# Performance work log

Measured on AMD Instinct MI355X. Metric: run time of the kernel, lower is better.

Reference implementation:

```python
import jax, jax.numpy as jnp
import numpy as np

DIM = 256
NUM_HEADS = 4
HEAD_DIM = DIM // NUM_HEADS
LN_EPS = 1e-5


def setup_inputs() -> dict:
    key = jax.random.key(0)
    ks = jax.random.split(key, 5)
    B, C, H, W = 4, DIM, 64, 64
    x = jax.random.normal(ks[0], (B, C, H, W), dtype=jnp.float32)
    ln_g = jnp.ones((DIM,), dtype=jnp.float32)
    ln_b = jnp.zeros((DIM,), dtype=jnp.float32)
    # torch Linear init scale ~ 1/sqrt(fan_in)
    w_qkv = jax.random.normal(ks[1], (DIM, 3 * DIM), dtype=jnp.float32) / np.sqrt(DIM)
    w_proj = jax.random.normal(ks[2], (DIM, DIM), dtype=jnp.float32) / np.sqrt(DIM)
    b_proj = jax.random.normal(ks[3], (DIM,), dtype=jnp.float32) * 0.01
    return {"x": x, "ln_g": ln_g, "ln_b": ln_b, "w_qkv": w_qkv,
            "w_proj": w_proj, "b_proj": b_proj}


def _attention_block(x, ln_g, ln_b, w_qkv, w_proj, b_proj):
    B, C, H, W = x.shape
    N = H * W
    h, d = NUM_HEADS, HEAD_DIM
    # b c h w -> b n c
    t = x.reshape(B, C, N).transpose(0, 2, 1)
    # LayerNorm over channel dim
    mu = jnp.mean(t, axis=-1, keepdims=True)
    var = jnp.mean(jnp.square(t - mu), axis=-1, keepdims=True)
    t = (t - mu) * jax.lax.rsqrt(var + LN_EPS) * ln_g + ln_b
    # qkv projection (no bias); layout of last dim is (three, heads, d)
    qkv = t @ w_qkv  # [B, N, 3*C]
    qkv = qkv.reshape(B, N, 3, h, d)
    q = qkv[:, :, 0].transpose(0, 2, 1, 3)  # [B, h, N, d]
    k = qkv[:, :, 1].transpose(0, 2, 1, 3)
    v = qkv[:, :, 2].transpose(0, 2, 1, 3)
    # scaled dot-product attention (original chunks over queries; same math)
    scale = 1.0 / jnp.sqrt(jnp.asarray(d, dtype=q.dtype))
    dots = jnp.einsum('bhnd,bhmd->bhnm', q, k) * scale
    attn = jax.nn.softmax(dots, axis=-1)
    o = jnp.einsum('bhnm,bhmd->bhnd', attn, v)  # [B, h, N, d]
    # b h n d -> b n (h d)
    o = o.transpose(0, 2, 1, 3).reshape(B, N, C)
    o = o @ w_proj.T + b_proj  # torch Linear convention not needed; keep explicit
    # b n c -> b c h w
    return o.transpose(0, 2, 1).reshape(B, C, H, W)


def reference(x, ln_g, ln_b, w_qkv, w_proj, b_proj):
    return _attention_block(x, ln_g, ln_b, w_qkv, w_proj, b_proj)
```

## Files before the change

kernel.cpp:

```cpp
#include <hip/hip_runtime.h>
#include <math.h>

#define NB 4
#define NC 256
#define NHEADS 4
#define DH 64
#define NT 4096
#define QSCALE (0.125f * 1.44269504088896f)

typedef __bf16  bf16x8 __attribute__((ext_vector_type(8)));
typedef __bf16  bf16x4 __attribute__((ext_vector_type(4)));
typedef float   f32x4  __attribute__((ext_vector_type(4)));
typedef short   s16x8  __attribute__((ext_vector_type(8)));

static __device__ __forceinline__ unsigned short f2bf(float f) {
    unsigned u = __float_as_uint(f);
    u = (u + 0x7fffu + ((u >> 16) & 1u)) >> 16;
    return (unsigned short)u;
}

static __device__ __forceinline__ void gload16(const unsigned short* g, unsigned short* l) {
    __builtin_amdgcn_global_load_lds((const __attribute__((address_space(1))) void*)g,
                                     (__attribute__((address_space(3))) void*)l, 16, 0, 0);
}

static __device__ __forceinline__ void stage_64x256(
    unsigned short* __restrict__ lds, const unsigned short* __restrict__ g, int tid)
{
    #pragma unroll
    for (int chunk = 0; chunk < 8; ++chunk) {
        const int row = chunk * 8 + (tid >> 5);
        const int col = (tid & 31) * 8;
        *(s16x8*)&lds[row * 264 + col] = *(const s16x8*)&g[row * 256 + col];
    }
}

__global__ __launch_bounds__(256) void k_prep(
    const float* __restrict__ wqkv, const float* __restrict__ wproj,
    unsigned short* __restrict__ wqkv_t, unsigned short* __restrict__ wproj_bf)
{
    const int id = blockIdx.x;
    const int tid = threadIdx.x;
    if (id < 48) {
        __shared__ float T[64][65];
        const int jt = id % 12, ct = id / 12;
        #pragma unroll
        for (int p = 0; p < 16; ++p) {
            const int idx = tid + (p << 8);
            const int r = idx >> 6, cl = idx & 63;
            T[r][cl] = wqkv[(size_t)(ct * 64 + r) * 768 + jt * 64 + cl];
        }
        __syncthreads();
        #pragma unroll
        for (int p = 0; p < 16; ++p) {
            const int idx = tid + (p << 8);
            const int r = idx >> 6, cl = idx & 63;
            wqkv_t[(size_t)(jt * 64 + r) * 256 + ct * 64 + cl] = f2bf(T[cl][r]);
        }
    } else {
        const int base = (id - 48) * 2048 + tid * 8;
        s16x8 v;
        #pragma unroll
        for (int j = 0; j < 8; ++j) v[j] = (short)f2bf(wproj[base + j]);
        *(s16x8*)&wproj_bf[base] = v;
    }
}

__global__ __launch_bounds__(256) void k_ln_qkv(
    const float* __restrict__ x,
    const float* __restrict__ ln_g,
    const float* __restrict__ ln_b,
    const unsigned short* __restrict__ wqkv_t,
    unsigned short* __restrict__ q_bf,
    unsigned short* __restrict__ k_bf,
    unsigned short* __restrict__ v_bf)
{
    __shared__ unsigned short An[64 * 264];
    __shared__ unsigned short Wt[64 * 264];
    __shared__ float red1[4][64], red2[4][64];
    __shared__ float mu_s[64], rs_s[64];

    const int b     = blockIdx.x >> 6;
    const int n0    = (blockIdx.x & 63) << 6;
    const int three = blockIdx.y;
    const int tid   = threadIdx.x;
    const int li    = tid & 63;
    const int grp   = tid >> 6;
    const int w     = grp;
    const int lane  = li;
    const int q4    = lane >> 4;
    const int c     = lane & 15;

    const float* xb = x + ((size_t)b * NC) * NT + n0 + li;

    float xr[64];
    #pragma unroll
    for (int chunk = 0; chunk < 8; ++chunk)
        #pragma unroll
        for (int j = 0; j < 8; ++j)
            xr[chunk * 8 + j] = xb[(size_t)(chunk * 32 + grp * 8 + j) * NT];

    float s1 = 0.f, s2 = 0.f;
    #pragma unroll
    for (int i = 0; i < 64; ++i) { s1 += xr[i]; s2 += xr[i] * xr[i]; }
    red1[grp][li] = s1; red2[grp][li] = s2;
    __syncthreads();
    if (tid < 64) {
        const float t1 = red1[0][tid] + red1[1][tid] + red1[2][tid] + red1[3][tid];
        const float t2 = red2[0][tid] + red2[1][tid] + red2[2][tid] + red2[3][tid];
        const float mu  = t1 * (1.0f / NC);
        const float var = t2 * (1.0f / NC) - mu * mu;
        mu_s[tid] = mu;
        rs_s[tid] = rsqrtf(var + 1e-5f);
    }
    __syncthreads();
    const float mu = mu_s[li];
    const float rs = rs_s[li];

    #pragma unroll
    for (int chunk = 0; chunk < 8; ++chunk) {
        s16x8 pk;
        #pragma unroll
        for (int j = 0; j < 8; ++j) {
            const int ch = chunk * 32 + grp * 8 + j;
            const float vv = (xr[chunk * 8 + j] - mu) * rs * ln_g[ch] + ln_b[ch];
            pk[j] = (short)f2bf(vv);
        }
        *(s16x8*)&An[li * 264 + chunk * 32 + grp * 8] = pk;
    }
    __syncthreads();

    bf16x8 aT[8];
    if (three < 2) {
        #pragma unroll
        for (int kt = 0; kt < 8; ++kt)
            aT[kt] = *(const bf16x8*)&An[(16 * w + c) * 264 + kt * 32 + q4 * 8];
    }

    for (int jt = 0; jt < 4; ++jt) {
        __syncthreads();
        stage_64x256(Wt, wqkv_t + (size_t)(three * 256 + jt * 64) * 256, tid);
        __syncthreads();

        f32x4 acc[4];
        #pragma unroll
        for (int nt = 0; nt < 4; ++nt)
            #pragma unroll
            for (int r = 0; r < 4; ++r) acc[nt][r] = 0.f;

        const int bh = b * NHEADS + jt;
        if (three < 2) {
            #pragma unroll
            for (int nt = 0; nt < 4; ++nt)
                #pragma unroll
                for (int kt = 0; kt < 8; ++kt) {
                    const bf16x8 bb = *(const bf16x8*)&Wt[(16 * nt + c) * 264 + kt * 32 + q4 * 8];
                    acc[nt] = __builtin_amdgcn_mfma_f32_16x16x32_bf16(aT[kt], bb, acc[nt], 0, 0, 0);
                }
            unsigned short* dst = (three == 0 ? q_bf : k_bf) + ((size_t)bh * NT + n0) * DH;
            const float sc = (three == 0) ? QSCALE : 1.0f;
            #pragma unroll
            for (int nt = 0; nt < 4; ++nt)
                #pragma unroll
                for (int r = 0; r < 4; ++r)
                    dst[(size_t)(16 * w + 4 * q4 + r) * DH + 16 * nt + c] = f2bf(acc[nt][r] * sc);
        } else {
            bf16x8 aW[8];
            #pragma unroll
            for (int kt = 0; kt < 8; ++kt)
                aW[kt] = *(const bf16x8*)&Wt[(16 * w + c) * 264 + kt * 32 + q4 * 8];
            #pragma unroll
            for (int nt = 0; nt < 4; ++nt)
                #pragma unroll
                for (int kt = 0; kt < 8; ++kt) {
                    const bf16x8 bb = *(const bf16x8*)&An[(16 * nt + c) * 264 + kt * 32 + q4 * 8];
                    acc[nt] = __builtin_amdgcn_mfma_f32_16x16x32_bf16(aW[kt], bb, acc[nt], 0, 0, 0);
                }
            unsigned short* dst = v_bf + (size_t)bh * DH * NT;
            #pragma unroll
            for (int nt = 0; nt < 4; ++nt)
                #pragma unroll
                for (int r = 0; r < 4; ++r)
                    dst[(size_t)(16 * w + 4 * q4 + r) * NT + n0 + 16 * nt + c] = f2bf(acc[nt][r]);
        }
    }
}

__global__ __launch_bounds__(256, 2) void k_attn(
    const unsigned short* __restrict__ qg,
    const unsigned short* __restrict__ kg,
    const unsigned short* __restrict__ vg,
    unsigned short* __restrict__ o)
{
    __shared__ unsigned short Ks[3 * 4096];
    __shared__ unsigned short Vt[3 * 4096];
    __shared__ __bf16 Ps[128 * 72];

    const int bh   = blockIdx.x >> 5;
    const int n0   = (blockIdx.x & 31) << 7;
    const int b    = bh >> 2;
    const int head = bh & 3;
    const int tid  = threadIdx.x;
    const int w    = tid >> 6;
    const int lane = tid & 63;
    const int q4   = lane >> 4;
    const int c    = lane & 15;

    const unsigned short* kb = kg + (size_t)bh * NT * DH;
    const unsigned short* vb = vg + (size_t)bh * DH * NT;

    bf16x8 aq[2][2];
    {
        const unsigned short* qp = qg + ((size_t)bh * NT + n0) * DH;
        #pragma unroll
        for (int g = 0; g < 2; ++g) {
            const unsigned short* qrow = qp + (size_t)(32 * w + 16 * g + c) * DH;
            aq[g][0] = *(const bf16x8*)(qrow + q4 * 8);
            aq[g][1] = *(const bf16x8*)(qrow + 32 + q4 * 8);
        }
    }

    const int rr = lane >> 3;
    const int kc = (lane & 7) ^ rr;
    const int koffK = rr * DH + kc * 8;

    const int sw0 = ((q4    ) ^ (c & 7)) * 8;
    const int sw1 = ((q4 + 4) ^ (c & 7)) * 8;

    #define ISSUE_TILE(it_, bi_)                                               \
        {                                                                      \
            const unsigned short* ktp = kb + (size_t)(it_) * 64 * DH;          \
            const unsigned short* vtp = vb + (size_t)(it_) * 64;               \
            _Pragma("unroll")                                                  \
            for (int t = 0; t < 2; ++t) {                                      \
                const int grp_ = w * 2 + t;                                    \
                gload16(ktp + grp_ * 512 + koffK,                              \
                        &Ks[(bi_) * 4096 + grp_ * 512 + lane * 8]);            \
                gload16(vtp + (size_t)(grp_ * 8 + rr) * NT + kc * 8,           \
                        &Vt[(bi_) * 4096 + grp_ * 512 + lane * 8]);            \
            }                                                                  \
        }

    ISSUE_TILE(0, 0)

    f32x4 oac[2][4];
    #pragma unroll
    for (int g = 0; g < 2; ++g)
        #pragma unroll
        for (int dt = 0; dt < 4; ++dt)
            #pragma unroll
            for (int r = 0; r < 4; ++r) oac[g][dt][r] = 0.f;
    float lsum[2][4] = {};

    int cur = 0, nxt = 1, nx2 = 2;
    for (int it = 0; it < 64; ++it) {
        if (it < 63) {
            ISSUE_TILE(it + 1, nxt)
            asm volatile("s_waitcnt vmcnt(4)\n\ts_barrier" ::: "memory");
        } else {
            asm volatile("s_waitcnt vmcnt(0)\n\ts_barrier" ::: "memory");
        }

        const unsigned short* Kb = &Ks[cur * 4096];
        const unsigned short* Vb = &Vt[cur * 4096];

        f32x4 st[2][4];
        #pragma unroll
        for (int nt = 0; nt < 4; ++nt) {
            const bf16x8 kf0 = *(const bf16x8*)&Kb[(16 * nt + c) * 64 + sw0];
            const bf16x8 kf1 = *(const bf16x8*)&Kb[(16 * nt + c) * 64 + sw1];
            #pragma unroll
            for (int g = 0; g < 2; ++g) {
                f32x4 acc;
                #pragma unroll
                for (int r = 0; r < 4; ++r) acc[r] = 0.f;
                acc = __builtin_amdgcn_mfma_f32_16x16x32_bf16(kf0, aq[g][0], acc, 0, 0, 0);
                acc = __builtin_amdgcn_mfma_f32_16x16x32_bf16(kf1, aq[g][1], acc, 0, 0, 0);
                st[g][nt] = acc;
            }
        }

        #pragma unroll
        for (int g = 0; g < 2; ++g)
            #pragma unroll
            for (int nt = 0; nt < 4; ++nt) {
                bf16x4 pk;
                #pragma unroll
                for (int r = 0; r < 4; ++r) {
                    const float e = exp2f(st[g][nt][r]);
                    lsum[g][nt] += e;
                    pk[r] = (__bf16)e;
                }
                *(bf16x4*)&Ps[(32 * w + 16 * g + c) * 72 + 16 * nt + 4 * q4] = pk;
            }

        bf16x8 pa[2][2];
        #pragma unroll
        for (int g = 0; g < 2; ++g) {
            const __bf16* prow = &Ps[(32 * w + 16 * g + c) * 72];
            pa[g][0] = *(const bf16x8*)(prow + q4 * 8);
            pa[g][1] = *(const bf16x8*)(prow + 32 + q4 * 8);
        }
        #pragma unroll
        for (int dt = 0; dt < 4; ++dt) {
            const bf16x8 v0 = *(const bf16x8*)&Vb[(16 * dt + c) * 64 + sw0];
            const bf16x8 v1 = *(const bf16x8*)&Vb[(16 * dt + c) * 64 + sw1];
            #pragma unroll
            for (int g = 0; g < 2; ++g) {
                oac[g][dt] = __builtin_amdgcn_mfma_f32_16x16x32_bf16(pa[g][0], v0, oac[g][dt], 0, 0, 0);
                oac[g][dt] = __builtin_amdgcn_mfma_f32_16x16x32_bf16(pa[g][1], v1, oac[g][dt], 0, 0, 0);
            }
        }

        const int tmp = cur; cur = nxt; nxt = nx2; nx2 = tmp;
    }
    #undef ISSUE_TILE

    float rinv[2][4];
    #pragma unroll
    for (int g = 0; g < 2; ++g) {
        float t = (lsum[g][0] + lsum[g][1]) + (lsum[g][2] + lsum[g][3]);
        t += __shfl_xor(t, 16);
        t += __shfl_xor(t, 32);
        #pragma unroll
        for (int r = 0; r < 4; ++r)
            rinv[g][r] = 1.0f / __shfl(t, 4 * q4 + r);
    }

    unsigned short* ob = o + ((size_t)b * NT + n0 + 32 * w) * NC + head * DH;
    #pragma unroll
    for (int g = 0; g < 2; ++g)
        #pragma unroll
        for (int dt = 0; dt < 4; ++dt)
            #pragma unroll
            for (int r = 0; r < 4; ++r)
                ob[(size_t)(16 * g + 4 * q4 + r) * NC + 16 * dt + c] =
                    f2bf(oac[g][dt][r] * rinv[g][r]);
}

__global__ __launch_bounds__(256) void k_proj(
    const unsigned short* __restrict__ o_bf,
    const unsigned short* __restrict__ wproj_bf,
    const float* __restrict__ b_proj,
    float* __restrict__ out)
{
    __shared__ unsigned short Os[64 * 264];
    __shared__ unsigned short Ws[64 * 264];

    const int b   = blockIdx.x >> 6;
    const int n0  = (blockIdx.x & 63) << 6;
    const int cg0 = blockIdx.y << 6;
    const int tid = threadIdx.x;
    const int w   = tid >> 6;
    const int lane = tid & 63;
    const int q4  = lane >> 4;
    const int c   = lane & 15;

    stage_64x256(Os, o_bf + ((size_t)b * NT + n0) * NC, tid);
    stage_64x256(Ws, wproj_bf + (size_t)cg0 * NC, tid);
    __syncthreads();

    bf16x8 a[8];
    #pragma unroll
    for (int kt = 0; kt < 8; ++kt)
        a[kt] = *(const bf16x8*)&Ws[(16 * w + c) * 264 + kt * 32 + q4 * 8];

    f32x4 acc[4];
    #pragma unroll
    for (int nt = 0; nt < 4; ++nt)
        #pragma unroll
        for (int r = 0; r < 4; ++r) acc[nt][r] = 0.f;

    #pragma unroll
    for (int nt = 0; nt < 4; ++nt)
        #pragma unroll
        for (int kt = 0; kt < 8; ++kt) {
            const bf16x8 bb = *(const bf16x8*)&Os[(16 * nt + c) * 264 + kt * 32 + q4 * 8];
            acc[nt] = __builtin_amdgcn_mfma_f32_16x16x32_bf16(a[kt], bb, acc[nt], 0, 0, 0);
        }

    #pragma unroll
    for (int nt = 0; nt < 4; ++nt)
        #pragma unroll
        for (int r = 0; r < 4; ++r) {
            const int cg = cg0 + 16 * w + 4 * q4 + r;
            out[((size_t)b * NC + cg) * NT + n0 + 16 * nt + c] = acc[nt][r] + b_proj[cg];
        }
}

extern "C" void kernel_launch(void* const* d_in, const int* in_sizes, int n_in,
                              void* d_out, int out_size, void* d_ws, size_t ws_size,
                              hipStream_t stream)
{
    const float* x      = (const float*)d_in[0];
    const float* ln_g   = (const float*)d_in[1];
    const float* ln_b   = (const float*)d_in[2];
    const float* w_qkv  = (const float*)d_in[3];
    const float* w_proj = (const float*)d_in[4];
    const float* b_proj = (const float*)d_in[5];
    float* out = (float*)d_out;

    const size_t TEN = (size_t)NB * NHEADS * NT * DH;

    unsigned short* ws16 = (unsigned short*)d_ws;
    unsigned short* q_bf    = ws16;
    unsigned short* k_bf    = ws16 + TEN;
    unsigned short* v_bf    = ws16 + 2 * TEN;
    unsigned short* o_bf    = ws16 + 3 * TEN;
    unsigned short* wqkv_t  = ws16 + 4 * TEN;
    unsigned short* wproj_b = wqkv_t + 768 * 256;

    k_prep<<<80, 256, 0, stream>>>(w_qkv, w_proj, wqkv_t, wproj_b);
    k_ln_qkv<<<dim3(NB * 64, 3), 256, 0, stream>>>(x, ln_g, ln_b, wqkv_t, q_bf, k_bf, v_bf);
    k_attn<<<16 * 32, 256, 0, stream>>>(q_bf, k_bf, v_bf, o_bf);
    k_proj<<<dim3(NB * 64, 4), 256, 0, stream>>>(o_bf, wproj_b, b_proj, out);
}
```

Measured before the change: 221.8 us.

## Split attention over two key halves and merge partials in projection kernel

The attention kernel now splits the key/value sequence into two halves per query tile, doubling the grid from 512 to 1024 blocks. It writes unnormalized fp32 partial outputs and row sums, which the projection kernel merges and normalizes while staging. The K/V shared-memory ring drops from triple to double buffering, with a full wait before each tile. This raises parallelism and occupancy on the many-CU device, at the cost of writing and reading large fp32 partials and less load/compute overlap.

Result: no change. 223.0 us (+0.5%).

```diff
diff --git a/kernel.cpp b/kernel.cpp
--- a/kernel.cpp
+++ b/kernel.cpp
@@ -190,24 +190,26 @@
     const unsigned short* __restrict__ qg,
     const unsigned short* __restrict__ kg,
     const unsigned short* __restrict__ vg,
-    unsigned short* __restrict__ o)
-{
-    __shared__ unsigned short Ks[3 * 4096];
-    __shared__ unsigned short Vt[3 * 4096];
+    float* __restrict__ o_part,
+    float* __restrict__ l_part)
+{
+    __shared__ unsigned short Ks[2 * 4096];
+    __shared__ unsigned short Vt[2 * 4096];
     __shared__ __bf16 Ps[128 * 72];
 
-    const int bh   = blockIdx.x >> 5;
-    const int n0   = (blockIdx.x & 31) << 7;
-    const int b    = bh >> 2;
-    const int head = bh & 3;
+    const int bh   = blockIdx.x >> 6;
+    const int rest = blockIdx.x & 63;
+    const int qt   = rest >> 1;
+    const int kh   = rest & 1;
+    const int n0   = qt << 7;
     const int tid  = threadIdx.x;
     const int w    = tid >> 6;
     const int lane = tid & 63;
     const int q4   = lane >> 4;
     const int c    = lane & 15;
 
-    const unsigned short* kb = kg + (size_t)bh * NT * DH;
-    const unsigned short* vb = vg + (size_t)bh * DH * NT;
+    const unsigned short* kb = kg + ((size_t)bh * NT + (kh << 11)) * DH;
+    const unsigned short* vb = vg + (size_t)bh * DH * NT + (kh << 11);
 
     bf16x8 aq[2][2];
     {
@@ -252,14 +254,10 @@
             for (int r = 0; r < 4; ++r) oac[g][dt][r] = 0.f;
     float lsum[2][4] = {};
 
-    int cur = 0, nxt = 1, nx2 = 2;
-    for (int it = 0; it < 64; ++it) {
-        if (it < 63) {
-            ISSUE_TILE(it + 1, nxt)
-            asm volatile("s_waitcnt vmcnt(4)\n\ts_barrier" ::: "memory");
-        } else {
-            asm volatile("s_waitcnt vmcnt(0)\n\ts_barrier" ::: "memory");
-        }
+    for (int it = 0; it < 32; ++it) {
+        const int cur = it & 1;
+        asm volatile("s_waitcnt vmcnt(0)\n\ts_barrier" ::: "memory");
+        if (it < 31) ISSUE_TILE(it + 1, cur ^ 1)
 
         const unsigned short* Kb = &Ks[cur * 4096];
         const unsigned short* Vb = &Vt[cur * 4096];
@@ -311,35 +309,31 @@
                 oac[g][dt] = __builtin_amdgcn_mfma_f32_16x16x32_bf16(pa[g][1], v1, oac[g][dt], 0, 0, 0);
             }
         }
-
-        const int tmp = cur; cur = nxt; nxt = nx2; nx2 = tmp;
     }
     #undef ISSUE_TILE
 
-    float rinv[2][4];
+    float* op = o_part + (((size_t)kh * 16 + bh) * NT + n0 + 32 * w) * DH;
+    #pragma unroll
+    for (int g = 0; g < 2; ++g)
+        #pragma unroll
+        for (int dt = 0; dt < 4; ++dt)
+            #pragma unroll
+            for (int r = 0; r < 4; ++r)
+                op[(size_t)(16 * g + 4 * q4 + r) * DH + 16 * dt + c] = oac[g][dt][r];
+
+    float* lp = l_part + ((size_t)kh * 16 + bh) * NT + n0 + 32 * w;
     #pragma unroll
     for (int g = 0; g < 2; ++g) {
         float t = (lsum[g][0] + lsum[g][1]) + (lsum[g][2] + lsum[g][3]);
         t += __shfl_xor(t, 16);
         t += __shfl_xor(t, 32);
-        #pragma unroll
-        for (int r = 0; r < 4; ++r)
-            rinv[g][r] = 1.0f / __shfl(t, 4 * q4 + r);
-    }
-
-    unsigned short* ob = o + ((size_t)b * NT + n0 + 32 * w) * NC + head * DH;
-    #pragma unroll
-    for (int g = 0; g < 2; ++g)
-        #pragma unroll
-        for (int dt = 0; dt < 4; ++dt)
-            #pragma unroll
-            for (int r = 0; r < 4; ++r)
-                ob[(size_t)(16 * g + 4 * q4 + r) * NC + 16 * dt + c] =
-                    f2bf(oac[g][dt][r] * rinv[g][r]);
+        if (q4 == 0) lp[16 * g + c] = t;
+    }
 }
 
 __global__ __launch_bounds__(256) void k_proj(
-    const unsigned short* __restrict__ o_bf,
+    const float* __restrict__ o_part,
+    const float* __restrict__ l_part,
     const unsigned short* __restrict__ wproj_bf,
     const float* __restrict__ b_proj,
     float* __restrict__ out)
@@ -356,7 +350,31 @@
     const int q4  = lane >> 4;
     const int c   = lane & 15;
 
-    stage_64x256(Os, o_bf + ((size_t)b * NT + n0) * NC, tid);
+    const size_t OPS = (size_t)16 * NT * DH;
+    const size_t LPS = (size_t)16 * NT;
+
+    #pragma unroll
+    for (int chunk = 0; chunk < 8; ++chunk) {
+        const int row = chunk * 8 + (tid >> 5);
+        const int col = (tid & 31) * 8;
+        const int hd  = col >> 6;
+        const int c64 = col & 63;
+        const size_t tok = (size_t)(b * NHEADS + hd) * NT + n0 + row;
+        const float rv = 1.0f / (l_part[tok] + l_part[LPS + tok]);
+        const float* p0 = o_part + tok * DH + c64;
+        const float* p1 = p0 + OPS;
+        const f32x4 a0 = *(const f32x4*)p0;
+        const f32x4 a1 = *(const f32x4*)(p0 + 4);
+        const f32x4 b0 = *(const f32x4*)p1;
+        const f32x4 b1 = *(const f32x4*)(p1 + 4);
+        s16x8 pk;
+        #pragma unroll
+        for (int j = 0; j < 4; ++j) {
+            pk[j]     = (short)f2bf((a0[j] + b0[j]) * rv);
+            pk[4 + j] = (short)f2bf((a1[j] + b1[j]) * rv);
+        }
+        *(s16x8*)&Os[row * 264 + col] = pk;
+    }
     stage_64x256(Ws, wproj_bf + (size_t)cg0 * NC, tid);
     __syncthreads();
 
@@ -402,16 +420,18 @@
 
     const size_t TEN = (size_t)NB * NHEADS * NT * DH;
 
-    unsigned short* ws16 = (unsigned short*)d_ws;
+    float* ws32 = (float*)d_ws;
+    float* o_part = ws32;
+    float* l_part = ws32 + 8388608;
+    unsigned short* ws16 = (unsigned short*)(l_part + 131072);
     unsigned short* q_bf    = ws16;
     unsigned short* k_bf    = ws16 + TEN;
     unsigned short* v_bf    = ws16 + 2 * TEN;
-    unsigned short* o_bf    = ws16 + 3 * TEN;
-    unsigned short* wqkv_t  = ws16 + 4 * TEN;
+    unsigned short* wqkv_t  = ws16 + 3 * TEN;
     unsigned short* wproj_b = wqkv_t + 768 * 256;
 
     k_prep<<<80, 256, 0, stream>>>(w_qkv, w_proj, wqkv_t, wproj_b);
     k_ln_qkv<<<dim3(NB * 64, 3), 256, 0, stream>>>(x, ln_g, ln_b, wqkv_t, q_bf, k_bf, v_bf);
-    k_attn<<<16 * 32, 256, 0, stream>>>(q_bf, k_bf, v_bf, o_bf);
-    k_proj<<<dim3(NB * 64, 4), 256, 0, stream>>>(o_bf, wproj_b, b_proj, out);
-}
+    k_attn<<<16 * 64, 256, 0, stream>>>(q_bf, k_bf, v_bf, o_part, l_part);
+    k_proj<<<dim3(NB * 64, 4), 256, 0, stream>>>(o_part, l_part, wproj_b, b_proj, out);
+}
```
